# Kernel optimization log

Hardware: AMD Instinct MI355X
Metric: run time of the kernel (lower is better)

Reference implementation:

```python
import jax, jax.numpy as jnp
import numpy as np

B, S, L, H, VIN, VOUT = 64, 64, 64, 256, 10000, 10000


def setup_inputs() -> dict:
    key = jax.random.key(0)
    ks = jax.random.split(key, 14)
    f = lambda k, shp: jax.random.normal(k, shp, dtype=jnp.float32) * 0.05
    return {
        "X": f(ks[0], (B, S, VIN)),
        "ground_truth": jax.random.randint(ks[1], (B, L), 0, VOUT, dtype=jnp.int32),
        "enc_Wih": f(ks[2], (3 * H, VIN)),
        "enc_Whh": f(ks[3], (3 * H, H)),
        "enc_bih": f(ks[4], (3 * H,)),
        "enc_bhh": f(ks[5], (3 * H,)),
        "att_w": f(ks[6], (2 * H,)),
        "att_b": f(ks[7], ()),
        "dec_Wih": f(ks[8], (3 * H, H + VOUT)),
        "dec_Whh": f(ks[9], (3 * H, H)),
        "dec_bih": f(ks[10], (3 * H,)),
        "dec_bhh": f(ks[11], (3 * H,)),
        "out_W": f(ks[12], (VOUT, H)),
        "out_b": f(ks[13], (VOUT,)),
    }


def gru_cell(h, x, Wih, Whh, bih, bhh):
    # PyTorch GRU cell: gates ordered (r, z, n)
    gi = x @ Wih.T + bih          # [B, 3H]
    gh = h @ Whh.T + bhh          # [B, 3H]
    ir, iz, inn = jnp.split(gi, 3, axis=-1)
    hr, hz, hn = jnp.split(gh, 3, axis=-1)
    r = jax.nn.sigmoid(ir + hr)
    z = jax.nn.sigmoid(iz + hz)
    n = jnp.tanh(inn + r * hn)
    return (1.0 - z) * n + z * h


def reference(X, ground_truth, enc_Wih, enc_Whh, enc_bih, enc_bhh,
              att_w, att_b, dec_Wih, dec_Whh, dec_bih, dec_bhh, out_W, out_b):
    b = X.shape[0]
    h_dim = enc_Whh.shape[1]
    vout = out_W.shape[0]

    # ---- encoder GRU over time (time-major scan) ----
    Xs = jnp.transpose(X, (1, 0, 2))                      # [S, B, VIN]
    h0 = jnp.zeros((b, h_dim), X.dtype)

    def enc_step(h, x):
        h2 = gru_cell(h, x, enc_Wih, enc_Whh, enc_bih, enc_bhh)
        return h2, h2

    h_last, enc_h = jax.lax.scan(enc_step, h0, Xs)        # enc_h: [S, B, H]

    # additive attention: logits = relu(W_a [h_dec; enc_h] + b_a)
    w_dec, w_enc = jnp.split(att_w, 2)                    # each [H]
    enc_score = jnp.einsum('sbh,h->sb', enc_h, w_enc)     # precomputed, [S, B]

    gtT = ground_truth.T                                  # [L, B]
    prev0 = jnp.zeros((b, vout), X.dtype)                 # initial one-hot input (zeros)

    def dec_step(carry, gt_i):
        h, prev = carry
        logits = jax.nn.relu(enc_score + h @ w_dec + att_b)   # [S, B]
        wts = jax.nn.softmax(logits, axis=0)                  # softmax over enc positions
        ctx = jnp.einsum('sb,sbh->bh', wts, enc_h)            # [B, H]
        dec_in = jnp.concatenate([ctx, prev], axis=-1)        # [B, H + VOUT]
        h2 = gru_cell(h, dec_in, dec_Wih, dec_Whh, dec_bih, dec_bhh)
        logp = jax.nn.log_softmax(h2 @ out_W.T + out_b, axis=-1)  # [B, VOUT]
        onehot = jax.nn.one_hot(gt_i, vout, dtype=X.dtype)        # teacher forcing
        return (h2, onehot), logp

    _, outs = jax.lax.scan(dec_step, (h_last, prev0), gtT)    # [L, B, VOUT]
    return jnp.transpose(outs, (1, 0, 2))                     # [B, L, VOUT]
```

## Files before the change

kernel.cpp:

```cpp
#include <hip/hip_runtime.h>
#include <hip/hip_bf16.h>
#include <math.h>

#define NB 64
#define NS 64
#define NL 64
#define NH 256
#define G3 768
#define NVIN 10000
#define NVOUT 10000
#define KP2 10240
#define NOUTP 10112

typedef __attribute__((ext_vector_type(8))) short bf16x8;
typedef __attribute__((ext_vector_type(4))) float f32x4;
typedef __attribute__((ext_vector_type(4))) unsigned int u32x4;

__device__ __forceinline__ void gld_lds16(const __hip_bfloat16* g, __hip_bfloat16* l) {
  __builtin_amdgcn_global_load_lds(
      (const __attribute__((address_space(1))) unsigned int*)(const void*)g,
      (__attribute__((address_space(3))) unsigned int*)(void*)l, 16, 0, 0);
}

__device__ __forceinline__ unsigned int f2bf(float f) {
  unsigned int u = __float_as_uint(f);
  return (u + 0x7fff + ((u >> 16) & 1)) >> 16;
}

__device__ __forceinline__ float fast_tanh(float x) {
  float e = __expf(-2.f * x);
  return (1.f - e) / (1.f + e);
}

__device__ __forceinline__ void lds_barrier() {
  asm volatile("s_waitcnt lgkmcnt(0)\n\ts_barrier" ::: "memory");
}

__global__ __launch_bounds__(256) void k_cvt_pad(
    const float* __restrict__ in, __hip_bfloat16* __restrict__ out,
    int in_rows, int in_cols, int out_cols, int swz) {
  int r = blockIdx.x;
  const float* src = in + (size_t)r * in_cols;
  __hip_bfloat16* dst = out + (size_t)r * out_cols;
  bool live = r < in_rows;
  int sx = swz ? ((r & 7) << 3) : 0;
  for (int c = threadIdx.x * 4; c < out_cols; c += 1024) {
    int cc = (c & ~63) | ((c & 63) ^ sx);
    __hip_bfloat16 v[4];
    if (live && cc + 3 < in_cols) {
      float4 f = *(const float4*)(src + cc);
      v[0] = __float2bfloat16(f.x); v[1] = __float2bfloat16(f.y);
      v[2] = __float2bfloat16(f.z); v[3] = __float2bfloat16(f.w);
    } else {
      v[0] = v[1] = v[2] = v[3] = __float2bfloat16(0.f);
    }
    *(ushort4*)(dst + c) = *(const ushort4*)v;
  }
}

__global__ __launch_bounds__(256) void k_wpack(
    const float* __restrict__ srcA, int strideA,
    const float* __restrict__ srcB, int strideB,
    __hip_bfloat16* __restrict__ out, int total) {
  int idx = blockIdx.x * 256 + threadIdx.x;
  if (idx >= total) return;
  int k = idx & 255, c = (idx >> 8) & 255, f = idx >> 16;
  float v = (f < 3) ? srcA[(size_t)(f * 256 + c) * strideA + k]
                    : srcB[(size_t)((f - 3) * 256 + c) * strideB + k];
  out[idx] = __float2bfloat16(v);
}

__global__ __launch_bounds__(256) void k_gemm_encS(
    const __hip_bfloat16* __restrict__ A, const __hip_bfloat16* __restrict__ B,
    float* __restrict__ P) {
  __shared__ __hip_bfloat16 As[128][64];
  __shared__ __hip_bfloat16 Bs[128][64];
  int t = threadIdx.x;
  int wid = t >> 6, lane = t & 63;
  int m0 = blockIdx.y * 128, n0 = blockIdx.x * 128;
  int wr = wid >> 1, wc = wid & 1;
  int r16 = lane & 15, hi16 = lane >> 4;
  int xr = (r16 & 7) << 4;
  f32x4 acc[4][4] = {};
  int kbeg = blockIdx.z * 2560;
  for (int ks = 0; ks < 40; ++ks) {
    int k0 = kbeg + ks * 64;
    __syncthreads();
#pragma unroll
    for (int is = 0; is < 4; ++is) {
      int off = is * 4096 + t * 16;
      int r = off >> 7, e = (off & 127) >> 1;
      gld_lds16(A + (size_t)(m0 + r) * KP2 + k0 + e, &As[r][e]);
      gld_lds16(B + (size_t)(n0 + r) * KP2 + k0 + e, &Bs[r][e]);
    }
    __syncthreads();
    const char* ab = (const char*)As;
    const char* bb = (const char*)Bs;
#pragma unroll
    for (int kk = 0; kk < 2; ++kk) {
      int ko = kk * 64 + hi16 * 16;
      bf16x8 af[4], bfr[4];
#pragma unroll
      for (int i = 0; i < 4; ++i) {
        af[i]  = *(const bf16x8*)(ab + (wr * 64 + i * 16 + r16) * 128 + (ko ^ xr));
        bfr[i] = *(const bf16x8*)(bb + (wc * 64 + i * 16 + r16) * 128 + (ko ^ xr));
      }
#pragma unroll
      for (int i = 0; i < 4; ++i)
#pragma unroll
        for (int j = 0; j < 4; ++j)
          acc[i][j] = __builtin_amdgcn_mfma_f32_16x16x32_bf16(af[i], bfr[j], acc[i][j], 0, 0, 0);
    }
  }
  float* Pz = P + (size_t)blockIdx.z * 4096 * G3;
#pragma unroll
  for (int i = 0; i < 4; ++i)
#pragma unroll
    for (int j = 0; j < 4; ++j) {
      int ccol = n0 + wc * 64 + j * 16 + r16;
#pragma unroll
      for (int q = 0; q < 4; ++q) {
        int crow = m0 + wr * 64 + i * 16 + hi16 * 4 + q;
        Pz[(size_t)crow * G3 + ccol] = acc[i][j][q];
      }
    }
}

__global__ __launch_bounds__(256) void k_reduce4(
    const float4* __restrict__ P, const float* __restrict__ bias,
    float4* __restrict__ G) {
  int idx = blockIdx.x * 256 + threadIdx.x;
  float4 a = P[idx], b = P[idx + 786432], c = P[idx + 2 * 786432],
         d = P[idx + 3 * 786432];
  float4 bs = *(const float4*)(bias + (idx % 192) * 4);
  float4 o;
  o.x = a.x + b.x + c.x + d.x + bs.x;
  o.y = a.y + b.y + c.y + d.y + bs.y;
  o.z = a.z + b.z + c.z + d.z + bs.z;
  o.w = a.w + b.w + c.w + d.w + bs.w;
  G[idx] = o;
}

__global__ __launch_bounds__(256) void k_gemm_outS(
    const __hip_bfloat16* __restrict__ A, const __hip_bfloat16* __restrict__ B,
    const float* __restrict__ bias, float* __restrict__ C) {
  __shared__ __hip_bfloat16 As[128][64];
  __shared__ __hip_bfloat16 Bs[128][64];
  int t = threadIdx.x;
  int wid = t >> 6, lane = t & 63;
  int m0 = blockIdx.y * 128, n0 = blockIdx.x * 128;
  int wr = wid >> 1, wc = wid & 1;
  int r16 = lane & 15, hi16 = lane >> 4;
  int xr = (r16 & 7) << 4;
  f32x4 acc[4][4] = {};
  for (int k0 = 0; k0 < NH; k0 += 64) {
    __syncthreads();
#pragma unroll
    for (int is = 0; is < 4; ++is) {
      int off = is * 4096 + t * 16;
      int r = off >> 7, e = (off & 127) >> 1;
      gld_lds16(A + (size_t)(m0 + r) * NH + k0 + e, &As[r][e]);
      gld_lds16(B + (size_t)(n0 + r) * NH + k0 + e, &Bs[r][e]);
    }
    __syncthreads();
    const char* ab = (const char*)As;
    const char* bb = (const char*)Bs;
#pragma unroll
    for (int kk = 0; kk < 2; ++kk) {
      int ko = kk * 64 + hi16 * 16;
      bf16x8 af[4], bfr[4];
#pragma unroll
      for (int i = 0; i < 4; ++i) {
        af[i]  = *(const bf16x8*)(ab + (wr * 64 + i * 16 + r16) * 128 + (ko ^ xr));
        bfr[i] = *(const bf16x8*)(bb + (wc * 64 + i * 16 + r16) * 128 + (ko ^ xr));
      }
#pragma unroll
      for (int i = 0; i < 4; ++i)
#pragma unroll
        for (int j = 0; j < 4; ++j)
          acc[i][j] = __builtin_amdgcn_mfma_f32_16x16x32_bf16(af[i], bfr[j], acc[i][j], 0, 0, 0);
    }
  }
#pragma unroll
  for (int i = 0; i < 4; ++i)
#pragma unroll
    for (int j = 0; j < 4; ++j) {
      int ccol = n0 + wc * 64 + j * 16 + r16;
      if (ccol < NVOUT) {
        float bs = bias[ccol];
#pragma unroll
        for (int q = 0; q < 4; ++q) {
          int crow = m0 + wr * 64 + i * 16 + hi16 * 4 + q;
          int l = crow >> 6, b = crow & 63;
          C[((size_t)b * NL + l) * NVOUT + ccol] = acc[i][j][q] + bs;
        }
      }
    }
}

__global__ __launch_bounds__(256) void k_gemm_encw(
    const __hip_bfloat16* __restrict__ A, const __hip_bfloat16* __restrict__ B,
    __hip_bfloat16* __restrict__ CT) {
  __shared__ __hip_bfloat16 As[128][32];
  __shared__ __hip_bfloat16 Bs[128][32];
  int t = threadIdx.x;
  int wid = t >> 6, lane = t & 63;
  int m0 = blockIdx.y * 128, n0 = blockIdx.x * 128;
  int wr = wid >> 1, wc = wid & 1;
  f32x4 acc[4][4] = {};
  for (int k0 = 0; k0 < NH; k0 += 32) {
    __syncthreads();
#pragma unroll
    for (int is = 0; is < 2; ++is) {
      int off = is * 4096 + wid * 1024 + lane * 16;
      int r = off >> 6, cb = (off & 63) >> 1;
      gld_lds16(A + (size_t)(m0 + r) * NH + k0 + cb, &As[r][cb]);
      gld_lds16(B + (size_t)(n0 + r) * NH + k0 + cb, &Bs[r][cb]);
    }
    __syncthreads();
    int r16 = lane & 15, kb = (lane >> 4) * 8;
    bf16x8 af[4], bfr[4];
#pragma unroll
    for (int i = 0; i < 4; ++i) {
      af[i]  = *(const bf16x8*)&As[wr * 64 + i * 16 + r16][kb];
      bfr[i] = *(const bf16x8*)&Bs[wc * 64 + i * 16 + r16][kb];
    }
#pragma unroll
    for (int i = 0; i < 4; ++i)
#pragma unroll
      for (int j = 0; j < 4; ++j)
        acc[i][j] = __builtin_amdgcn_mfma_f32_16x16x32_bf16(af[i], bfr[j], acc[i][j], 0, 0, 0);
  }
  int r16 = lane & 15, rg = lane >> 4;
#pragma unroll
  for (int i = 0; i < 4; ++i)
#pragma unroll
    for (int j = 0; j < 4; ++j) {
      int ccol = n0 + wc * 64 + j * 16 + r16;
#pragma unroll
      for (int q = 0; q < 4; ++q) {
        int crow = m0 + wr * 64 + i * 16 + rg * 4 + q;
        int bb = crow >> 6, ss = crow & 63;
        CT[((size_t)bb * G3 + ccol) * 64 + (ss ^ ((ccol & 7) << 3))] =
            __float2bfloat16(acc[i][j][q]);
      }
    }
}

__global__ __launch_bounds__(256) void k_pregather(
    const float* __restrict__ Wih, const float* __restrict__ bih,
    const int* __restrict__ gt, float* __restrict__ Gdec) {
  int ib = blockIdx.x;
  int i = ib >> 6, b = ib & 63;
  int tok = (i > 0) ? gt[b * NL + (i - 1)] : -1;
  for (int g = threadIdx.x; g < G3; g += 256) {
    float v = bih[g];
    if (tok >= 0) v += Wih[(size_t)g * (NH + NVOUT) + NH + tok];
    Gdec[(size_t)ib * G3 + g] = v;
  }
}

__global__ __launch_bounds__(512) void k_encoder5(
    const float* __restrict__ Gi, const __hip_bfloat16* __restrict__ Wcat,
    const float* __restrict__ bhh, __hip_bfloat16* __restrict__ enchB) {
  __shared__ __hip_bfloat16 hbf[2][256];
  int t = threadIdx.x, w = t >> 6, lane = t & 63;
  int b = blockIdx.x;
  int r16 = lane & 15, hi16 = lane >> 4;
  int cw = w * 32;
  bf16x8 wv[3][2][8];
#pragma unroll
  for (int f = 0; f < 3; ++f)
#pragma unroll
    for (int fc = 0; fc < 2; ++fc)
#pragma unroll
      for (int kf = 0; kf < 8; ++kf)
        wv[f][fc][kf] = *(const bf16x8*)(Wcat +
            (((size_t)f * 256 + cw + fc * 16 + r16) * 256 + kf * 32 + hi16 * 8));
  float bh0[2], bh1[2], bh2[2];
#pragma unroll
  for (int fc = 0; fc < 2; ++fc) {
    bh0[fc] = bhh[cw + fc * 16 + r16];
    bh1[fc] = bhh[256 + cw + fc * 16 + r16];
    bh2[fc] = bhh[512 + cw + fc * 16 + r16];
  }
  if (t < 256) {
    hbf[0][t] = __float2bfloat16(0.f);
    hbf[1][t] = __float2bfloat16(0.f);
  }
  __syncthreads();
  float hp[2] = {0.f, 0.f};
  int cur = 0;
  for (int s = 0; s < NS; ++s) {
    float gd0[2], gd1[2], gd2[2];
    if (hi16 == 0) {
      const float* gp = Gi + ((size_t)b * 64 + s) * G3;
#pragma unroll
      for (int fc = 0; fc < 2; ++fc) {
        gd0[fc] = gp[cw + fc * 16 + r16];
        gd1[fc] = gp[256 + cw + fc * 16 + r16];
        gd2[fc] = gp[512 + cw + fc * 16 + r16];
      }
    }
    const char* hb = (const char*)&hbf[cur][0];
    f32x4 acc[3][2] = {};
#pragma unroll
    for (int half = 0; half < 2; ++half) {
      bf16x8 ah[4];
#pragma unroll
      for (int kf = 0; kf < 4; ++kf)
        ah[kf] = *(const bf16x8*)(hb + (half * 4 + kf) * 64 + hi16 * 16);
#pragma unroll
      for (int f = 0; f < 3; ++f)
#pragma unroll
        for (int fc = 0; fc < 2; ++fc)
#pragma unroll
          for (int kf = 0; kf < 4; ++kf)
            acc[f][fc] = __builtin_amdgcn_mfma_f32_16x16x32_bf16(
                ah[kf], wv[f][fc][half * 4 + kf], acc[f][fc], 0, 0, 0);
    }
    if (hi16 == 0) {
      int nxt = cur ^ 1;
#pragma unroll
      for (int fc = 0; fc < 2; ++fc) {
        int c = cw + fc * 16 + r16;
        float rr = 1.f / (1.f + __expf(-(gd0[fc] + acc[0][fc][0] + bh0[fc])));
        float zz = 1.f / (1.f + __expf(-(gd1[fc] + acc[1][fc][0] + bh1[fc])));
        float nn = fast_tanh(gd2[fc] + rr * (acc[2][fc][0] + bh2[fc]));
        float hn = (1.f - zz) * nn + zz * hp[fc];
        hp[fc] = hn;
        hbf[nxt][c] = __float2bfloat16(hn);
        enchB[((size_t)b * 64 + s) * 256 + c] = __float2bfloat16(hn);
      }
    }
    lds_barrier();
    cur ^= 1;
  }
}

__global__ __launch_bounds__(256) void k_escoreB(
    const __hip_bfloat16* __restrict__ enchB, const float* __restrict__ att_w,
    float* __restrict__ escoreT) {
  int row = blockIdx.x * 4 + (threadIdx.x >> 6);
  int lane = threadIdx.x & 63;
  ushort4 u = *(const ushort4*)(enchB + (size_t)row * 256 + lane * 4);
  const float* we = att_w + 256 + lane * 4;
  float p = __uint_as_float((unsigned)u.x << 16) * we[0]
          + __uint_as_float((unsigned)u.y << 16) * we[1]
          + __uint_as_float((unsigned)u.z << 16) * we[2]
          + __uint_as_float((unsigned)u.w << 16) * we[3];
#pragma unroll
  for (int off = 32; off; off >>= 1) p += __shfl_xor(p, off, 64);
  if (lane == 0) escoreT[row] = p;
}

__global__ __launch_bounds__(512) void k_decoder7(
    const float* __restrict__ Gdec, const __hip_bfloat16* __restrict__ Wcat6,
    const float* __restrict__ bhh, const __hip_bfloat16* __restrict__ enchB,
    const __hip_bfloat16* __restrict__ ENCWT, const float* __restrict__ escoreT,
    const float* __restrict__ att_w, const float* __restrict__ att_b,
    __hip_bfloat16* __restrict__ dechb) {
  __shared__ __hip_bfloat16 encwT[G3 + 8][64];
  __shared__ __hip_bfloat16 hbf[2][256];
  __shared__ float psumL[2][8];
  int t = threadIdx.x, w = t >> 6, lane = t & 63;
  int b = blockIdx.x;
  int r16 = lane & 15, hi16 = lane >> 4;
  int cw = w * 32;
  {
    const char* srcb = (const char*)(ENCWT + (size_t)b * G3 * 64);
    char* dstb = (char*)&encwT[0][0];
#pragma unroll
    for (int is = 0; is < 12; ++is) {
      int off = is * 8192 + t * 16;
      gld_lds16((const __hip_bfloat16*)(srcb + off), (__hip_bfloat16*)(dstb + off));
    }
  }
  {
    unsigned* op = (unsigned*)&encwT[768][0];
    if (t < 32) op[t] = 0x3F803F80u;
  }
  bf16x8 wv[3][2][8];
#pragma unroll
  for (int f = 0; f < 3; ++f)
#pragma unroll
    for (int fc = 0; fc < 2; ++fc)
#pragma unroll
      for (int kf = 0; kf < 8; ++kf)
        wv[f][fc][kf] = *(const bf16x8*)(Wcat6 +
            (((size_t)(3 + f) * 256 + cw + fc * 16 + r16) * 256 + kf * 32 + hi16 * 8));
  float wd0 = att_w[cw + r16], wd1 = att_w[cw + 16 + r16];
  float attb = att_b[0];
  float esc = escoreT[(size_t)b * 64 + lane];
  float bh0[2], bh1[2], bh2[2];
#pragma unroll
  for (int fc = 0; fc < 2; ++fc) {
    bh0[fc] = bhh[cw + fc * 16 + r16];
    bh1[fc] = bhh[256 + cw + fc * 16 + r16];
    bh2[fc] = bhh[512 + cw + fc * 16 + r16];
  }
  if (t < 256) {
    hbf[0][t] = enchB[((size_t)b * 64 + 63) * 256 + t];
    hbf[1][t] = __float2bfloat16(0.f);
  }
  float hp[2];
  hp[0] = __bfloat162float(enchB[((size_t)b * 64 + 63) * 256 + cw + r16]);
  hp[1] = __bfloat162float(enchB[((size_t)b * 64 + 63) * 256 + cw + 16 + r16]);
  if (hi16 == 0) {
    float pp = hp[0] * wd0 + hp[1] * wd1;
    pp += __shfl_xor(pp, 1, 64); pp += __shfl_xor(pp, 2, 64);
    pp += __shfl_xor(pp, 4, 64); pp += __shfl_xor(pp, 8, 64);
    if (lane == 0) psumL[0][w] = pp;
  }
  __syncthreads();
  int bs3 = (b & 7) << 3;
  int cur = 0;
  for (int i = 0; i < NL; ++i) {
    float gd0[2], gd1[2], gd2[2];
    if (hi16 == 0) {
      const float* gp = Gdec + ((size_t)i * 64 + b) * G3;
#pragma unroll
      for (int fc = 0; fc < 2; ++fc) {
        gd0[fc] = gp[cw + fc * 16 + r16];
        gd1[fc] = gp[256 + cw + fc * 16 + r16];
        gd2[fc] = gp[512 + cw + fc * 16 + r16];
      }
    }
    const char* hb = (const char*)&hbf[cur][0];
    bf16x8 ah[8];
#pragma unroll
    for (int kf = 0; kf < 8; ++kf)
      ah[kf] = *(const bf16x8*)(hb + kf * 64 + hi16 * 16);
    float4 pa = *(const float4*)&psumL[cur][0];
    float4 pb = *(const float4*)&psumL[cur][4];
    float p = ((pa.x + pa.y) + (pa.z + pa.w)) + ((pb.x + pb.y) + (pb.z + pb.w));
    f32x4 acch[3][2] = {};
#pragma unroll
    for (int f = 0; f < 3; ++f)
#pragma unroll
      for (int fc = 0; fc < 2; ++fc)
#pragma unroll
        for (int kf = 0; kf < 8; ++kf)
          acch[f][fc] = __builtin_amdgcn_mfma_f32_16x16x32_bf16(
              ah[kf], wv[f][fc][kf], acch[f][fc], 0, 0, 0);
    float lg = fmaxf(esc + p + attb, 0.f);
    float e = __expf(lg);
    bf16x8 af_[2];
#pragma unroll
    for (int kf = 0; kf < 2; ++kf) {
      u32x4 tmp;
#pragma unroll
      for (int j = 0; j < 4; ++j) {
        int src = hi16 * 8 + kf * 32 + 2 * j;
        tmp[j] = f2bf(__shfl(e, src, 64)) | (f2bf(__shfl(e, src + 1, 64)) << 16);
      }
      af_[kf] = __builtin_bit_cast(bf16x8, tmp);
    }
    f32x4 acci[3][2] = {};
    f32x4 accs = {};
    const char* eb = (const char*)&encwT[0][0];
#pragma unroll
    for (int g = 0; g < 3; ++g)
#pragma unroll
      for (int fc = 0; fc < 2; ++fc) {
        int cloc = g * 256 + cw + fc * 16 + r16;
        int xb = (cloc & 7) << 4;
#pragma unroll
        for (int kf = 0; kf < 2; ++kf) {
          bf16x8 bfrag = *(const bf16x8*)(eb + cloc * 128 + ((kf * 64 + hi16 * 16) ^ xb));
          acci[g][fc] = __builtin_amdgcn_mfma_f32_16x16x32_bf16(
              af_[kf], bfrag, acci[g][fc], 0, 0, 0);
        }
      }
#pragma unroll
    for (int kf = 0; kf < 2; ++kf) {
      bf16x8 ofrag = *(const bf16x8*)(eb + 768 * 128 + kf * 64 + hi16 * 16);
      accs = __builtin_amdgcn_mfma_f32_16x16x32_bf16(af_[kf], ofrag, accs, 0, 0, 0);
    }
    if (hi16 == 0) {
      float rn = 1.f / accs[0];
      int nxt = cur ^ 1;
      float hn2[2];
#pragma unroll
      for (int fc = 0; fc < 2; ++fc) {
        int c = cw + fc * 16 + r16;
        float rr = 1.f / (1.f + __expf(-(gd0[fc] + acci[0][fc][0] * rn + acch[0][fc][0] + bh0[fc])));
        float zz = 1.f / (1.f + __expf(-(gd1[fc] + acci[1][fc][0] * rn + acch[1][fc][0] + bh1[fc])));
        float nn = fast_tanh(gd2[fc] + acci[2][fc][0] * rn + rr * (acch[2][fc][0] + bh2[fc]));
        float hn = (1.f - zz) * nn + zz * hp[fc];
        hp[fc] = hn; hn2[fc] = hn;
        hbf[nxt][c] = __float2bfloat16(hn);
        int cs = (c & ~63) | ((c & 63) ^ bs3);
        dechb[((size_t)i * 64 + b) * 256 + cs] = __float2bfloat16(hn);
      }
      float pp = hn2[0] * wd0 + hn2[1] * wd1;
      pp += __shfl_xor(pp, 1, 64); pp += __shfl_xor(pp, 2, 64);
      pp += __shfl_xor(pp, 4, 64); pp += __shfl_xor(pp, 8, 64);
      if (lane == 0) psumL[cur ^ 1][w] = pp;
    }
    lds_barrier();
    cur ^= 1;
  }
}

__global__ __launch_bounds__(256) void k_logsoftmax(float* __restrict__ out) {
  float* x = out + (size_t)blockIdx.x * NVOUT;
  __shared__ float red[256];
  int t = threadIdx.x;
  float4 v[10];
  float mx = -1e30f;
#pragma unroll
  for (int ii = 0; ii < 10; ++ii) {
    int slot = ii * 256 + t;
    if (slot < 2500) {
      v[ii] = *(const float4*)(x + slot * 4);
      mx = fmaxf(mx, fmaxf(fmaxf(v[ii].x, v[ii].y), fmaxf(v[ii].z, v[ii].w)));
    }
  }
  red[t] = mx; __syncthreads();
  for (int off = 128; off; off >>= 1) {
    if (t < off) red[t] = fmaxf(red[t], red[t + off]);
    __syncthreads();
  }
  mx = red[0]; __syncthreads();
  float sm = 0.f;
#pragma unroll
  for (int ii = 0; ii < 10; ++ii) {
    int slot = ii * 256 + t;
    if (slot < 2500)
      sm += __expf(v[ii].x - mx) + __expf(v[ii].y - mx)
          + __expf(v[ii].z - mx) + __expf(v[ii].w - mx);
  }
  red[t] = sm; __syncthreads();
  for (int off = 128; off; off >>= 1) {
    if (t < off) red[t] += red[t + off];
    __syncthreads();
  }
  float lse = mx + logf(red[0]);
#pragma unroll
  for (int ii = 0; ii < 10; ++ii) {
    int slot = ii * 256 + t;
    if (slot < 2500) {
      float4 o; o.x = v[ii].x - lse; o.y = v[ii].y - lse;
      o.z = v[ii].z - lse; o.w = v[ii].w - lse;
      *(float4*)(x + slot * 4) = o;
    }
  }
}

extern "C" void kernel_launch(void* const* d_in, const int* in_sizes, int n_in,
                              void* d_out, int out_size, void* d_ws, size_t ws_size,
                              hipStream_t stream) {
  const float* X        = (const float*)d_in[0];
  const int*   gt       = (const int*)  d_in[1];
  const float* enc_Wih  = (const float*)d_in[2];
  const float* enc_Whh  = (const float*)d_in[3];
  const float* enc_bih  = (const float*)d_in[4];
  const float* enc_bhh  = (const float*)d_in[5];
  const float* att_w    = (const float*)d_in[6];
  const float* att_b    = (const float*)d_in[7];
  const float* dec_Wih  = (const float*)d_in[8];
  const float* dec_Whh  = (const float*)d_in[9];
  const float* dec_bih  = (const float*)d_in[10];
  const float* dec_bhh  = (const float*)d_in[11];
  const float* out_W    = (const float*)d_in[12];
  const float* out_b    = (const float*)d_in[13];
  float* out = (float*)d_out;

  float* p = (float*)d_ws;
  float* Gienc  = p; p += NS * NB * G3;
  float* Gdec   = p; p += NL * NB * G3;
  float* escoreT = p; p += NB * NS;
  __hip_bfloat16* q = (__hip_bfloat16*)p;
  __hip_bfloat16* enchBb = q; q += (size_t)NB * NS * NH;
  __hip_bfloat16* Wcat_e = q; q += (size_t)3 * 256 * 256;
  __hip_bfloat16* Wcat_d = q; q += (size_t)6 * 256 * 256;
  __hip_bfloat16* Xb     = q; q += (size_t)4096 * KP2;
  __hip_bfloat16* Wencb  = q; q += (size_t)G3 * KP2;
  __hip_bfloat16* Woutb  = q; q += (size_t)NOUTP * NH;
  __hip_bfloat16* dechb  = q; q += (size_t)NL * NB * NH;
  __hip_bfloat16* ENCWT  = (__hip_bfloat16*)Gienc;
  float* Pout = (float*)d_out;

  k_cvt_pad<<<4096, 256, 0, stream>>>(X, Xb, 4096, NVIN, KP2, 1);
  k_cvt_pad<<<G3, 256, 0, stream>>>(enc_Wih, Wencb, G3, NVIN, KP2, 1);
  k_cvt_pad<<<NOUTP, 256, 0, stream>>>(out_W, Woutb, NVOUT, NH, NH, 1);
  k_wpack<<<768, 256, 0, stream>>>(enc_Whh, NH, enc_Whh, NH, Wcat_e, 3 * 65536);
  k_wpack<<<1536, 256, 0, stream>>>(dec_Wih, NH + NVOUT, dec_Whh, NH, Wcat_d, 6 * 65536);
  k_pregather<<<NL * NB, 256, 0, stream>>>(dec_Wih, dec_bih, gt, Gdec);

  k_gemm_encS<<<dim3(6, 32, 4), 256, 0, stream>>>(Xb, Wencb, Pout);
  k_reduce4<<<3072, 256, 0, stream>>>((const float4*)Pout, enc_bih, (float4*)Gienc);
  k_encoder5<<<64, 512, 0, stream>>>(Gienc, Wcat_e, enc_bhh, enchBb);
  k_escoreB<<<1024, 256, 0, stream>>>(enchBb, att_w, escoreT);
  k_gemm_encw<<<dim3(6, 32), 256, 0, stream>>>(enchBb, Wcat_d, ENCWT);
  k_decoder7<<<64, 512, 0, stream>>>(Gdec, Wcat_d, dec_bhh, enchBb, ENCWT,
                                     escoreT, att_w, att_b, dechb);
  k_gemm_outS<<<dim3(79, 32), 256, 0, stream>>>(dechb, Woutb, out_b, out);
  k_logsoftmax<<<NB * NL, 256, 0, stream>>>(out);
}
```

Measured before the change: 733.8 us.

## Replace per-step attention matmul with sorted prefix-sum tables over ReLU threshold

The attention logits are relu(escore + d), where d is a per-step scalar. The softmax-weighted context projection can therefore be written as exp(d)·P[m] + Q[m], where m counts the positions above the threshold. A new kernel sorts the encoder scores per batch row and precomputes prefix tables of exp-weighted and plain sums of the projected encoder states. Each decoder step then does a ballot and popcount plus a few table loads instead of an MFMA over a 64×768 LDS tile. This removes the large LDS staging and the per-step attention MFMAs from the serial decoder loop, but adds an extra kernel, global loads on the critical path, and bf16 rounding of the prefix sums. The rewrite also leaves dead code (the unused gi0/gi1 values) and loads tp/tq redundantly.

```diff
diff --git a/kernel.cpp b/kernel.cpp
--- a/kernel.cpp
+++ b/kernel.cpp
@@ -200,7 +200,7 @@
 
 __global__ __launch_bounds__(256) void k_gemm_encw(
     const __hip_bfloat16* __restrict__ A, const __hip_bfloat16* __restrict__ B,
-    __hip_bfloat16* __restrict__ CT) {
+    __hip_bfloat16* __restrict__ C) {
   __shared__ __hip_bfloat16 As[128][32];
   __shared__ __hip_bfloat16 Bs[128][32];
   int t = threadIdx.x;
@@ -240,11 +240,63 @@
 #pragma unroll
       for (int q = 0; q < 4; ++q) {
         int crow = m0 + wr * 64 + i * 16 + rg * 4 + q;
-        int bb = crow >> 6, ss = crow & 63;
-        CT[((size_t)bb * G3 + ccol) * 64 + (ss ^ ((ccol & 7) << 3))] =
-            __float2bfloat16(acc[i][j][q]);
-      }
-    }
+        C[(size_t)crow * G3 + ccol] = __float2bfloat16(acc[i][j][q]);
+      }
+    }
+}
+
+__global__ __launch_bounds__(256) void k_tabs(
+    const __hip_bfloat16* __restrict__ ENCW, const float* __restrict__ escoreT,
+    __hip_bfloat16* __restrict__ TP, __hip_bfloat16* __restrict__ TQ,
+    float* __restrict__ thrG, float* __restrict__ sigG) {
+  __shared__ float thrL[64];
+  __shared__ int   idxL[64];
+  __shared__ float wexpL[64];
+  int b = blockIdx.x, t = threadIdx.x;
+  if (t < 64) {
+    float mine = escoreT[b * 64 + t];
+    int rank = 0;
+    for (int j = 0; j < 64; ++j) {
+      float v = __shfl(mine, j, 64);
+      rank += (v > mine) || (v == mine && j < t);
+    }
+    thrL[rank] = mine;
+    idxL[rank] = t;
+  }
+  __syncthreads();
+  if (t < 64) {
+    float e = __expf(thrL[t]);
+    wexpL[t] = e;
+    float s = e;
+    for (int off = 1; off < 64; off <<= 1) {
+      float o = __shfl_up(s, off, 64);
+      if (t >= off) s += o;
+    }
+    sigG[b * 65 + t + 1] = s;
+    if (t == 0) sigG[b * 65] = 0.f;
+    thrG[b * 64 + t] = thrL[t];
+  }
+  __syncthreads();
+#pragma unroll
+  for (int cc = 0; cc < 3; ++cc) {
+    int c = t + cc * 256;
+    const __hip_bfloat16* ep = ENCW + (size_t)b * 64 * G3 + c;
+    float T = 0.f;
+    for (int s = 0; s < 64; ++s) T += __bfloat162float(ep[(size_t)s * G3]);
+    float P = 0.f, U = 0.f;
+    __hip_bfloat16* tp = TP + (size_t)b * 65 * G3 + c;
+    __hip_bfloat16* tq = TQ + (size_t)b * 65 * G3 + c;
+    tp[0] = __float2bfloat16(0.f);
+    tq[0] = __float2bfloat16(T);
+    for (int m = 1; m <= 64; ++m) {
+      int j = idxL[m - 1];
+      float e = __bfloat162float(ep[(size_t)j * G3]);
+      P += wexpL[m - 1] * e;
+      U += e;
+      tp[(size_t)m * G3] = __float2bfloat16(P);
+      tq[(size_t)m * G3] = __float2bfloat16(T - U);
+    }
+  }
 }
 
 __global__ __launch_bounds__(256) void k_pregather(
@@ -354,32 +406,20 @@
   if (lane == 0) escoreT[row] = p;
 }
 
-__global__ __launch_bounds__(512) void k_decoder7(
+__global__ __launch_bounds__(512) void k_decoder8(
     const float* __restrict__ Gdec, const __hip_bfloat16* __restrict__ Wcat6,
     const float* __restrict__ bhh, const __hip_bfloat16* __restrict__ enchB,
-    const __hip_bfloat16* __restrict__ ENCWT, const float* __restrict__ escoreT,
+    const __hip_bfloat16* __restrict__ TP, const __hip_bfloat16* __restrict__ TQ,
+    const float* __restrict__ thrG, const float* __restrict__ sigG,
     const float* __restrict__ att_w, const float* __restrict__ att_b,
     __hip_bfloat16* __restrict__ dechb) {
-  __shared__ __hip_bfloat16 encwT[G3 + 8][64];
   __shared__ __hip_bfloat16 hbf[2][256];
   __shared__ float psumL[2][8];
+  __shared__ float sigL[65];
   int t = threadIdx.x, w = t >> 6, lane = t & 63;
   int b = blockIdx.x;
   int r16 = lane & 15, hi16 = lane >> 4;
   int cw = w * 32;
-  {
-    const char* srcb = (const char*)(ENCWT + (size_t)b * G3 * 64);
-    char* dstb = (char*)&encwT[0][0];
-#pragma unroll
-    for (int is = 0; is < 12; ++is) {
-      int off = is * 8192 + t * 16;
-      gld_lds16((const __hip_bfloat16*)(srcb + off), (__hip_bfloat16*)(dstb + off));
-    }
-  }
-  {
-    unsigned* op = (unsigned*)&encwT[768][0];
-    if (t < 32) op[t] = 0x3F803F80u;
-  }
   bf16x8 wv[3][2][8];
 #pragma unroll
   for (int f = 0; f < 3; ++f)
@@ -391,7 +431,8 @@
             (((size_t)(3 + f) * 256 + cw + fc * 16 + r16) * 256 + kf * 32 + hi16 * 8));
   float wd0 = att_w[cw + r16], wd1 = att_w[cw + 16 + r16];
   float attb = att_b[0];
-  float esc = escoreT[(size_t)b * 64 + lane];
+  float thr = thrG[(size_t)b * 64 + lane];
+  if (t < 65) sigL[t] = sigG[(size_t)b * 65 + t];
   float bh0[2], bh1[2], bh2[2];
 #pragma unroll
   for (int fc = 0; fc < 2; ++fc) {
@@ -413,6 +454,8 @@
     if (lane == 0) psumL[0][w] = pp;
   }
   __syncthreads();
+  const __hip_bfloat16* tpb = TP + (size_t)b * 65 * G3;
+  const __hip_bfloat16* tqb = TQ + (size_t)b * 65 * G3;
   int bs3 = (b & 7) << 3;
   int cur = 0;
   for (int i = 0; i < NL; ++i) {
@@ -426,14 +469,25 @@
         gd2[fc] = gp[512 + cw + fc * 16 + r16];
       }
     }
+    float4 pa = *(const float4*)&psumL[cur][0];
+    float4 pb = *(const float4*)&psumL[cur][4];
+    float d = ((pa.x + pa.y) + (pa.z + pa.w)) + ((pb.x + pb.y) + (pb.z + pb.w)) + attb;
+    float ed = __expf(d);
+    unsigned long long bal = __ballot(thr + d > 0.f);
+    int m = __popcll(bal);
+    float tp0 = 0.f, tp1 = 0.f, tq0 = 0.f, tq1 = 0.f, sg = 0.f;
+    if (hi16 == 0) {
+      const __hip_bfloat16* tpr = tpb + (size_t)m * G3 + cw + r16;
+      const __hip_bfloat16* tqr = tqb + (size_t)m * G3 + cw + r16;
+      tp0 = __bfloat162float(tpr[0]);  tp1 = __bfloat162float(tpr[16]);
+      tq0 = __bfloat162float(tqr[0]);  tq1 = __bfloat162float(tqr[16]);
+      sg = sigL[m];
+    }
     const char* hb = (const char*)&hbf[cur][0];
     bf16x8 ah[8];
 #pragma unroll
     for (int kf = 0; kf < 8; ++kf)
       ah[kf] = *(const bf16x8*)(hb + kf * 64 + hi16 * 16);
-    float4 pa = *(const float4*)&psumL[cur][0];
-    float4 pb = *(const float4*)&psumL[cur][4];
-    float p = ((pa.x + pa.y) + (pa.z + pa.w)) + ((pb.x + pb.y) + (pb.z + pb.w));
     f32x4 acch[3][2] = {};
 #pragma unroll
     for (int f = 0; f < 3; ++f)
@@ -443,50 +497,39 @@
         for (int kf = 0; kf < 8; ++kf)
           acch[f][fc] = __builtin_amdgcn_mfma_f32_16x16x32_bf16(
               ah[kf], wv[f][fc][kf], acch[f][fc], 0, 0, 0);
-    float lg = fmaxf(esc + p + attb, 0.f);
-    float e = __expf(lg);
-    bf16x8 af_[2];
-#pragma unroll
-    for (int kf = 0; kf < 2; ++kf) {
-      u32x4 tmp;
-#pragma unroll
-      for (int j = 0; j < 4; ++j) {
-        int src = hi16 * 8 + kf * 32 + 2 * j;
-        tmp[j] = f2bf(__shfl(e, src, 64)) | (f2bf(__shfl(e, src + 1, 64)) << 16);
-      }
-      af_[kf] = __builtin_bit_cast(bf16x8, tmp);
-    }
-    f32x4 acci[3][2] = {};
-    f32x4 accs = {};
-    const char* eb = (const char*)&encwT[0][0];
-#pragma unroll
-    for (int g = 0; g < 3; ++g)
-#pragma unroll
-      for (int fc = 0; fc < 2; ++fc) {
-        int cloc = g * 256 + cw + fc * 16 + r16;
-        int xb = (cloc & 7) << 4;
-#pragma unroll
-        for (int kf = 0; kf < 2; ++kf) {
-          bf16x8 bfrag = *(const bf16x8*)(eb + cloc * 128 + ((kf * 64 + hi16 * 16) ^ xb));
-          acci[g][fc] = __builtin_amdgcn_mfma_f32_16x16x32_bf16(
-              af_[kf], bfrag, acci[g][fc], 0, 0, 0);
-        }
-      }
-#pragma unroll
-    for (int kf = 0; kf < 2; ++kf) {
-      bf16x8 ofrag = *(const bf16x8*)(eb + 768 * 128 + kf * 64 + hi16 * 16);
-      accs = __builtin_amdgcn_mfma_f32_16x16x32_bf16(af_[kf], ofrag, accs, 0, 0, 0);
-    }
     if (hi16 == 0) {
-      float rn = 1.f / accs[0];
+      float rn = 1.f / (ed * sg + (float)(64 - m));
+      float gi0 = (ed * tp0 + tq0) * rn;
+      float gi1 = (ed * tp1 + tq1) * rn;
       int nxt = cur ^ 1;
       float hn2[2];
 #pragma unroll
       for (int fc = 0; fc < 2; ++fc) {
         int c = cw + fc * 16 + r16;
-        float rr = 1.f / (1.f + __expf(-(gd0[fc] + acci[0][fc][0] * rn + acch[0][fc][0] + bh0[fc])));
-        float zz = 1.f / (1.f + __expf(-(gd1[fc] + acci[1][fc][0] * rn + acch[1][fc][0] + bh1[fc])));
-        float nn = fast_tanh(gd2[fc] + acci[2][fc][0] * rn + rr * (acch[2][fc][0] + bh2[fc]));
+        float gi = fc ? gi1 : gi0;
+        (void)gi;
+        (void)c;
+      }
+      float tpr0[2], tpz0[2], tpn0[2], tqr0[2], tqz0[2], tqn0[2];
+#pragma unroll
+      for (int fc = 0; fc < 2; ++fc) {
+        int c = cw + fc * 16 + r16;
+        tpr0[fc] = __bfloat162float(tpb[(size_t)m * G3 + c]);
+        tpz0[fc] = __bfloat162float(tpb[(size_t)m * G3 + 256 + c]);
+        tpn0[fc] = __bfloat162float(tpb[(size_t)m * G3 + 512 + c]);
+        tqr0[fc] = __bfloat162float(tqb[(size_t)m * G3 + c]);
+        tqz0[fc] = __bfloat162float(tqb[(size_t)m * G3 + 256 + c]);
+        tqn0[fc] = __bfloat162float(tqb[(size_t)m * G3 + 512 + c]);
+      }
+#pragma unroll
+      for (int fc = 0; fc < 2; ++fc) {
+        int c = cw + fc * 16 + r16;
+        float gir = (ed * tpr0[fc] + tqr0[fc]) * rn;
+        float giz = (ed * tpz0[fc] + tqz0[fc]) * rn;
+        float gin = (ed * tpn0[fc] + tqn0[fc]) * rn;
+        float rr = 1.f / (1.f + __expf(-(gd0[fc] + gir + acch[0][fc][0] + bh0[fc])));
+        float zz = 1.f / (1.f + __expf(-(gd1[fc] + giz + acch[1][fc][0] + bh1[fc])));
+        float nn = fast_tanh(gd2[fc] + gin + rr * (acch[2][fc][0] + bh2[fc]));
         float hn = (1.f - zz) * nn + zz * hp[fc];
         hp[fc] = hn; hn2[fc] = hn;
         hbf[nxt][c] = __float2bfloat16(hn);
@@ -579,7 +622,11 @@
   __hip_bfloat16* Wencb  = q; q += (size_t)G3 * KP2;
   __hip_bfloat16* Woutb  = q; q += (size_t)NOUTP * NH;
   __hip_bfloat16* dechb  = q; q += (size_t)NL * NB * NH;
-  __hip_bfloat16* ENCWT  = (__hip_bfloat16*)Gienc;
+  __hip_bfloat16* ENCW   = (__hip_bfloat16*)Gienc;
+  __hip_bfloat16* TP  = Xb;
+  __hip_bfloat16* TQ  = Xb + (size_t)64 * 65 * G3;
+  float* thrG = (float*)(Xb + (size_t)2 * 64 * 65 * G3);
+  float* sigG = thrG + 64 * 64;
   float* Pout = (float*)d_out;
 
   k_cvt_pad<<<4096, 256, 0, stream>>>(X, Xb, 4096, NVIN, KP2, 1);
@@ -593,9 +640,10 @@
   k_reduce4<<<3072, 256, 0, stream>>>((const float4*)Pout, enc_bih, (float4*)Gienc);
   k_encoder5<<<64, 512, 0, stream>>>(Gienc, Wcat_e, enc_bhh, enchBb);
   k_escoreB<<<1024, 256, 0, stream>>>(enchBb, att_w, escoreT);
-  k_gemm_encw<<<dim3(6, 32), 256, 0, stream>>>(enchBb, Wcat_d, ENCWT);
-  k_decoder7<<<64, 512, 0, stream>>>(Gdec, Wcat_d, dec_bhh, enchBb, ENCWT,
-                                     escoreT, att_w, att_b, dechb);
+  k_gemm_encw<<<dim3(6, 32), 256, 0, stream>>>(enchBb, Wcat_d, ENCW);
+  k_tabs<<<64, 256, 0, stream>>>(ENCW, escoreT, TP, TQ, thrG, sigG);
+  k_decoder8<<<64, 512, 0, stream>>>(Gdec, Wcat_d, dec_bhh, enchBb, TP, TQ,
+                                     thrG, sigG, att_w, att_b, dechb);
   k_gemm_outS<<<dim3(79, 32), 256, 0, stream>>>(dechb, Woutb, out_b, out);
   k_logsoftmax<<<NB * NL, 256, 0, stream>>>(out);
 }
```

New measurement: 713.9 us. 2.7% less time.
